# Optimization experiments

Hardware: AMD Instinct MI355X
Metric: run time of the kernel (lower is better)

Reference implementation:

```python
import jax, jax.numpy as jnp
import numpy as np

H = 4            # heads
C = 64           # per-head dim (= hidden, PyG TransformerConv semantics)
HD = 64          # hidden_dim
L = 2            # num_layers
NT = 2           # node types: 0=task, 1=machine
ET = ((0, 1), (1, 0))  # edge types: (src_nt, dst_nt)
N = 16384        # nodes per type (== max_nodes -> simple pos-enc slice)
E = 262144       # edges per edge type


def _ln(x, g, b):
    mu = x.mean(-1, keepdims=True)
    var = ((x - mu) ** 2).mean(-1, keepdims=True)
    return (x - mu) * jax.lax.rsqrt(var + 1e-5) * g + b


def _tconv(x_src, x_dst, ei, Wq, bq, Wk, bk, Wv, bv, Ws, bs, Wb):
    # PyG TransformerConv: heads=H, out_channels=C, concat=False, beta=True
    n_dst = x_dst.shape[0]
    src, dst = ei[0], ei[1]
    q = (x_dst @ Wq + bq).reshape(-1, H, C)
    k = (x_src @ Wk + bk).reshape(-1, H, C)
    v = (x_src @ Wv + bv).reshape(-1, H, C)
    logits = jnp.einsum('ehc,ehc->eh', q[dst], k[src]) * (1.0 / float(np.sqrt(C)))  # [E,H]
    m = jax.ops.segment_max(logits, dst, num_segments=n_dst)          # [N,H] segment softmax
    ex = jnp.exp(logits - m[dst])
    denom = jax.ops.segment_sum(ex, dst, num_segments=n_dst)
    alpha = ex / denom[dst]                                            # [E,H]
    msg = (alpha[:, :, None] * v[src]).reshape(-1, H * C)              # [E,H*C]
    out = jax.ops.segment_sum(msg, dst, num_segments=n_dst)
    out = out.reshape(n_dst, H, C).mean(axis=1)                        # concat=False -> head mean
    r = x_dst @ Ws + bs                                                # lin_skip
    beta = jax.nn.sigmoid(jnp.concatenate([out, r, out - r], -1) @ Wb) # lin_beta, [N,1]
    return beta * r + (1.0 - beta) * out


def _forward(edge_index, x, W_in, b_in, type_emb, pos, Wq, bq, Wk, bk, Wv, bv,
             Wskip, bskip, Wbeta, ln_g, ln_b, ff_W1, ff_b1, ff_W2, ff_b2, W_out, b_out):
    # input proj + type embedding + positional encoding (num_nodes == max_nodes -> slice)
    h = [x[t] @ W_in[t] + b_in[t] + type_emb[t] + pos[t] for t in range(NT)]
    for l in range(L):
        hn = [jnp.zeros_like(h[0]), jnp.zeros_like(h[1])]
        for e, (s, d) in enumerate(ET):  # HeteroConv, aggr='sum'
            hn[d] = hn[d] + _tconv(h[s], h[d], edge_index[e],
                                   Wq[l, e], bq[l, e], Wk[l, e], bk[l, e],
                                   Wv[l, e], bv[l, e], Wskip[l, e], bskip[l, e], Wbeta[l, e])
        for t in range(NT):
            hr = _ln(h[t] + hn[t], ln_g[l, t], ln_b[l, t])
            ff = jax.nn.gelu(hr @ ff_W1[l, t] + ff_b1[l, t], approximate=False) @ ff_W2[l, t] + ff_b2[l, t]
            h[t] = hr + ff
    return jnp.stack([h[t] @ W_out[t] + b_out[t] for t in range(NT)])  # [NT,N,HD]


def setup_inputs() -> dict:
    key = jax.random.key(0)
    ks = jax.random.split(key, 16)
    w = lambda k, s: 0.02 * jax.random.normal(k, s, jnp.float32)
    NE = len(ET)
    return {
        'x': jax.random.normal(ks[0], (NT, N, HD), jnp.float32),
        'edge_index': jax.random.randint(ks[1], (NE, 2, E), 0, N, jnp.int32),
        'W_in': w(ks[2], (NT, HD, HD)), 'b_in': jnp.zeros((NT, HD), jnp.float32),
        'type_emb': w(ks[3], (NT, HD)),
        'pos': w(ks[4], (NT, N, HD)),
        'Wq': w(ks[5], (L, NE, HD, H * C)), 'bq': jnp.zeros((L, NE, H * C), jnp.float32),
        'Wk': w(ks[6], (L, NE, HD, H * C)), 'bk': jnp.zeros((L, NE, H * C), jnp.float32),
        'Wv': w(ks[7], (L, NE, HD, H * C)), 'bv': jnp.zeros((L, NE, H * C), jnp.float32),
        'Wskip': w(ks[8], (L, NE, HD, HD)), 'bskip': jnp.zeros((L, NE, HD), jnp.float32),
        'Wbeta': w(ks[9], (L, NE, 3 * HD, 1)),
        'ln_g': jnp.ones((L, NT, HD), jnp.float32), 'ln_b': jnp.zeros((L, NT, HD), jnp.float32),
        'ff_W1': w(ks[10], (L, NT, HD, 4 * HD)), 'ff_b1': jnp.zeros((L, NT, 4 * HD), jnp.float32),
        'ff_W2': w(ks[11], (L, NT, 4 * HD, HD)), 'ff_b2': jnp.zeros((L, NT, HD), jnp.float32),
        'W_out': w(ks[12], (NT, HD, HD)), 'b_out': jnp.zeros((NT, HD), jnp.float32),
    }


def reference(x, edge_index, W_in, b_in, type_emb, pos, Wq, bq, Wk, bk, Wv, bv,
              Wskip, bskip, Wbeta, ln_g, ln_b, ff_W1, ff_b1, ff_W2, ff_b2, W_out, b_out):
    return _forward(edge_index, x, W_in, b_in, type_emb, pos, Wq, bq, Wk, bk, Wv, bv,
                    Wskip, bskip, Wbeta, ln_g, ln_b, ff_W1, ff_b1, ff_W2, ff_b2, W_out, b_out)
```

## Files before the change

### kernel.cpp

```cpp
#include <hip/hip_runtime.h>
#include <math.h>

#define NN 16384
#define EE 262144

typedef __bf16 v8bf __attribute__((ext_vector_type(8)));
typedef __bf16 v4bf __attribute__((ext_vector_type(4)));
typedef float  v4f  __attribute__((ext_vector_type(4)));
typedef float  v2f  __attribute__((ext_vector_type(2)));

#define OFF_CNT     0
#define OFF_FILL    (2*NN)
#define OFF_ROWPTR  (4*NN)
#define OFF_COLSRC  98816
#define OFF_H       623104
#define OFF_HN      (OFF_H  + 2*NN*64)
#define OFF_Q       (OFF_HN + 2*NN*64)
#define OFF_KV      (OFF_Q  + 2*NN*128)
#define OFF_R       (OFF_KV + 2*NN*128)

__device__ __forceinline__ float blo(unsigned u) { return __uint_as_float(u << 16); }
__device__ __forceinline__ float bhi(unsigned u) { return __uint_as_float(u & 0xffff0000u); }
__device__ __forceinline__ unsigned short f2b(float f) {
  __bf16 h = (__bf16)f;
  return *(unsigned short*)&h;
}

__global__ void count_kernel(const int* __restrict__ ei, int* __restrict__ cnt) {
  int idx = blockIdx.x * 256 + threadIdx.x;
  if (idx >= 2 * EE) return;
  int et = idx >> 18;
  int j  = idx & (EE - 1);
  int dst = ei[et * 2 * EE + EE + j];
  atomicAdd(&cnt[et * NN + dst], 1);
}

__global__ __launch_bounds__(1024) void scan_kernel(const int* __restrict__ cnt,
                                                    int* __restrict__ rowptr,
                                                    int* __restrict__ fill) {
  int et = blockIdx.x;
  const int* c = cnt + et * NN;
  __shared__ int sums[1024];
  int tid = threadIdx.x;
  int base = tid * 16;
  int loc[16];
  int s = 0;
#pragma unroll
  for (int i = 0; i < 16; ++i) { loc[i] = s; s += c[base + i]; }
  sums[tid] = s;
  __syncthreads();
  for (int off = 1; off < 1024; off <<= 1) {
    int v = 0;
    if (tid >= off) v = sums[tid - off];
    __syncthreads();
    if (tid >= off) sums[tid] += v;
    __syncthreads();
  }
  int ebase = (tid == 0) ? 0 : sums[tid - 1];
  int* rp = rowptr + et * (NN + 1);
  int* fl = fill + et * NN;
#pragma unroll
  for (int i = 0; i < 16; ++i) {
    rp[base + i] = ebase + loc[i];
    fl[base + i] = ebase + loc[i];
  }
  if (tid == 1023) rp[NN] = sums[1023];
}

__global__ void scatter_kernel(const int* __restrict__ ei, int* __restrict__ fill,
                               int* __restrict__ colsrc) {
  int idx = blockIdx.x * 256 + threadIdx.x;
  if (idx >= 2 * EE) return;
  int et = idx >> 18;
  int j  = idx & (EE - 1);
  int src = ei[et * 2 * EE + j];
  int dst = ei[et * 2 * EE + EE + j];
  int pos = atomicAdd(&fill[et * NN + dst], 1);
  colsrc[et * EE + pos] = (et * NN + src) << 9;
}

struct GemmDesc {
  const float *A, *B, *bias, *bias2, *add;
  char* C;
  int Ncols, Cld, ntiles, gelu, otype;
};
struct GemmPack { GemmDesc d[8]; int nd; };

#define LDA 72

__global__ __launch_bounds__(256) void gemm_mfma(GemmPack p) {
  GemmDesc g = p.d[blockIdx.y];
  const int row0 = blockIdx.x * 128;
  const int tid = threadIdx.x;
  const int w = tid >> 6, lane = tid & 63;
  const int l16 = lane & 15, quad = lane >> 4;

  __shared__ __bf16 As[128 * LDA];
  __shared__ __bf16 Bs[64 * LDA];

#pragma unroll
  for (int it = 0; it < 8; ++it) {
    int fi = it * 256 + tid;
    int grow = fi >> 4;
    int kq = (fi & 15) << 2;
    float4 a = *(const float4*)(g.A + (size_t)(row0 + grow) * 64 + kq);
    v4bf c = { (__bf16)a.x, (__bf16)a.y, (__bf16)a.z, (__bf16)a.w };
    *(v4bf*)&As[grow * LDA + kq] = c;
  }

  for (int ct0 = 0; ct0 < g.ntiles; ++ct0) {
    const int col0 = ct0 * 64;
    __syncthreads();
#pragma unroll
    for (int it = 0; it < 4; ++it) {
      int fi = it * 256 + tid;
      int kk = fi >> 4;
      int nq = (fi & 15) << 2;
      float4 b = *(const float4*)(g.B + (size_t)kk * g.Ncols + col0 + nq);
      Bs[(nq + 0) * LDA + kk] = (__bf16)b.x;
      Bs[(nq + 1) * LDA + kk] = (__bf16)b.y;
      Bs[(nq + 2) * LDA + kk] = (__bf16)b.z;
      Bs[(nq + 3) * LDA + kk] = (__bf16)b.w;
    }
    __syncthreads();

    v4f acc[2][4];
#pragma unroll
    for (int rt = 0; rt < 2; ++rt)
#pragma unroll
      for (int ct = 0; ct < 4; ++ct)
#pragma unroll
        for (int r = 0; r < 4; ++r) acc[rt][ct][r] = 0.f;

#pragma unroll
    for (int ks = 0; ks < 2; ++ks) {
      v8bf a0 = *(v8bf*)&As[(w * 32 + l16) * LDA + ks * 32 + quad * 8];
      v8bf a1 = *(v8bf*)&As[(w * 32 + 16 + l16) * LDA + ks * 32 + quad * 8];
#pragma unroll
      for (int ct = 0; ct < 4; ++ct) {
        v8bf bb = *(v8bf*)&Bs[(ct * 16 + l16) * LDA + ks * 32 + quad * 8];
        acc[0][ct] = __builtin_amdgcn_mfma_f32_16x16x32_bf16(a0, bb, acc[0][ct], 0, 0, 0);
        acc[1][ct] = __builtin_amdgcn_mfma_f32_16x16x32_bf16(a1, bb, acc[1][ct], 0, 0, 0);
      }
    }

    float bias_c[4];
#pragma unroll
    for (int ct = 0; ct < 4; ++ct) {
      int col = col0 + ct * 16 + l16;
      float b = g.bias ? g.bias[col] : 0.f;
      if (g.bias2) b += g.bias2[col];
      bias_c[ct] = b;
    }
#pragma unroll
    for (int rt = 0; rt < 2; ++rt)
#pragma unroll
      for (int r = 0; r < 4; ++r) {
        size_t row = row0 + w * 32 + rt * 16 + quad * 4 + r;
        char* cp = g.C + row * (size_t)g.Cld;
#pragma unroll
        for (int ct = 0; ct < 4; ++ct) {
          int col = col0 + ct * 16 + l16;
          float v = acc[rt][ct][r] + bias_c[ct];
          if (g.add) v += g.add[row * g.Ncols + col];
          if (g.gelu) v = 0.5f * v * (1.f + erff(v * 0.70710678118654752f));
          if (g.otype == 0)      *(float*)(cp + col * 4) = v;
          else if (g.otype == 1) *(unsigned short*)(cp + col * 2) = f2b(v);
          else {
            unsigned pk = __builtin_amdgcn_cvt_pk_fp8_f32(v, v, 0, false);
            *(unsigned char*)(cp + col) = (unsigned char)(pk & 0xff);
          }
        }
      }
  }
}

struct FFPack {
  const float *HN, *W1, *b1, *W2, *b2;
  float* H;
  const float *Wout, *bout;
  float* outbuf;
};

__global__ __launch_bounds__(256) void ff_fused(FFPack p) {
  const int t = blockIdx.y;
  const int row0 = blockIdx.x * 64;
  const int tid = threadIdx.x;
  const int w = tid >> 6, lane = tid & 63;
  const int l16 = lane & 15, quad = lane >> 4;

  const float* A  = p.HN + ((size_t)t * NN) * 64;
  const float* W1 = p.W1 + (size_t)t * 64 * 256;
  const float* b1 = p.b1 + t * 256;
  const float* W2 = p.W2 + (size_t)t * 256 * 64;
  const float* b2 = p.b2 + t * 64;

  __shared__ __bf16 As[64 * LDA];
  __shared__ __bf16 A2[64 * LDA];
  __shared__ __bf16 B1s[64 * LDA];
  __shared__ __bf16 B2s[64 * LDA];

#pragma unroll
  for (int it = 0; it < 4; ++it) {
    int fi = it * 256 + tid;
    int grow = fi >> 4;
    int kq = (fi & 15) << 2;
    float4 a = *(const float4*)(A + (size_t)(row0 + grow) * 64 + kq);
    v4bf c = { (__bf16)a.x, (__bf16)a.y, (__bf16)a.z, (__bf16)a.w };
    *(v4bf*)&As[grow * LDA + kq] = c;
  }

  v4f acc2[4];
#pragma unroll
  for (int ct = 0; ct < 4; ++ct)
#pragma unroll
    for (int r = 0; r < 4; ++r) acc2[ct][r] = 0.f;

  for (int c1 = 0; c1 < 4; ++c1) {
#pragma unroll
    for (int it = 0; it < 4; ++it) {
      int fi = it * 256 + tid;
      int kk = fi >> 4;
      int nq = (fi & 15) << 2;
      float4 b = *(const float4*)(W1 + (size_t)kk * 256 + c1 * 64 + nq);
      B1s[(nq + 0) * LDA + kk] = (__bf16)b.x;
      B1s[(nq + 1) * LDA + kk] = (__bf16)b.y;
      B1s[(nq + 2) * LDA + kk] = (__bf16)b.z;
      B1s[(nq + 3) * LDA + kk] = (__bf16)b.w;
      float4 b2v = *(const float4*)(W2 + (size_t)(c1 * 64 + kk) * 64 + nq);
      B2s[(nq + 0) * LDA + kk] = (__bf16)b2v.x;
      B2s[(nq + 1) * LDA + kk] = (__bf16)b2v.y;
      B2s[(nq + 2) * LDA + kk] = (__bf16)b2v.z;
      B2s[(nq + 3) * LDA + kk] = (__bf16)b2v.w;
    }
    __syncthreads();

    v4f acc1[4];
#pragma unroll
    for (int ct = 0; ct < 4; ++ct)
#pragma unroll
      for (int r = 0; r < 4; ++r) acc1[ct][r] = 0.f;
#pragma unroll
    for (int ks = 0; ks < 2; ++ks) {
      v8bf a = *(v8bf*)&As[(w * 16 + l16) * LDA + ks * 32 + quad * 8];
#pragma unroll
      for (int ct = 0; ct < 4; ++ct) {
        v8bf bb = *(v8bf*)&B1s[(ct * 16 + l16) * LDA + ks * 32 + quad * 8];
        acc1[ct] = __builtin_amdgcn_mfma_f32_16x16x32_bf16(a, bb, acc1[ct], 0, 0, 0);
      }
    }
#pragma unroll
    for (int ct = 0; ct < 4; ++ct) {
      float bb = b1[c1 * 64 + ct * 16 + l16];
#pragma unroll
      for (int r = 0; r < 4; ++r) {
        float v = acc1[ct][r] + bb;
        v = 0.5f * v * (1.f + erff(v * 0.70710678118654752f));
        A2[(w * 16 + quad * 4 + r) * LDA + ct * 16 + l16] = (__bf16)v;
      }
    }
#pragma unroll
    for (int ks = 0; ks < 2; ++ks) {
      v8bf a = *(v8bf*)&A2[(w * 16 + l16) * LDA + ks * 32 + quad * 8];
#pragma unroll
      for (int ct = 0; ct < 4; ++ct) {
        v8bf bb = *(v8bf*)&B2s[(ct * 16 + l16) * LDA + ks * 32 + quad * 8];
        acc2[ct] = __builtin_amdgcn_mfma_f32_16x16x32_bf16(a, bb, acc2[ct], 0, 0, 0);
      }
    }
    __syncthreads();
  }

  if (!p.outbuf) {
#pragma unroll
    for (int ct = 0; ct < 4; ++ct) {
      int col = ct * 16 + l16;
      float bb = b2[col];
#pragma unroll
      for (int r = 0; r < 4; ++r) {
        size_t row = (size_t)t * NN + row0 + w * 16 + quad * 4 + r;
        float v = acc2[ct][r] + bb + p.HN[row * 64 + col];
        p.H[row * 64 + col] = v;
      }
    }
    return;
  }

#pragma unroll
  for (int ct = 0; ct < 4; ++ct) {
    int col = ct * 16 + l16;
    float bb = b2[col];
#pragma unroll
    for (int r = 0; r < 4; ++r) {
      int lrow = w * 16 + quad * 4 + r;
      size_t row = (size_t)t * NN + row0 + lrow;
      float v = acc2[ct][r] + bb + p.HN[row * 64 + col];
      A2[lrow * LDA + col] = (__bf16)v;
    }
  }
  {
    const float* Wo = p.Wout + (size_t)t * 64 * 64;
#pragma unroll
    for (int it = 0; it < 4; ++it) {
      int fi = it * 256 + tid;
      int kk = fi >> 4;
      int nq = (fi & 15) << 2;
      float4 b = *(const float4*)(Wo + (size_t)kk * 64 + nq);
      B1s[(nq + 0) * LDA + kk] = (__bf16)b.x;
      B1s[(nq + 1) * LDA + kk] = (__bf16)b.y;
      B1s[(nq + 2) * LDA + kk] = (__bf16)b.z;
      B1s[(nq + 3) * LDA + kk] = (__bf16)b.w;
    }
  }
  __syncthreads();

  v4f acc3[4];
#pragma unroll
  for (int ct = 0; ct < 4; ++ct)
#pragma unroll
    for (int r = 0; r < 4; ++r) acc3[ct][r] = 0.f;
#pragma unroll
  for (int ks = 0; ks < 2; ++ks) {
    v8bf a = *(v8bf*)&A2[(w * 16 + l16) * LDA + ks * 32 + quad * 8];
#pragma unroll
    for (int ct = 0; ct < 4; ++ct) {
      v8bf bb = *(v8bf*)&B1s[(ct * 16 + l16) * LDA + ks * 32 + quad * 8];
      acc3[ct] = __builtin_amdgcn_mfma_f32_16x16x32_bf16(a, bb, acc3[ct], 0, 0, 0);
    }
  }
  const float* bo = p.bout + t * 64;
#pragma unroll
  for (int ct = 0; ct < 4; ++ct) {
    int col = ct * 16 + l16;
    float bb = bo[col];
#pragma unroll
    for (int r = 0; r < 4; ++r) {
      size_t row = (size_t)t * NN + row0 + w * 16 + quad * 4 + r;
      p.outbuf[row * 64 + col] = acc3[ct][r] + bb;
    }
  }
}

struct AggPack {
  const unsigned short *Q;
  const char *KV;
  const float *R;
  const float *Wb;
  const float *Hin;
  const float *lng, *lnb;
  float* outHR;
  const int *rowptr;
  const int *colsrc;
};

__global__ __launch_bounds__(256) void agg_kernel(AggPack p) {
  const int et = blockIdx.y, d = 1 - et;
  int wid = __builtin_amdgcn_readfirstlane(threadIdx.x >> 6);
  int lane = threadIdx.x & 63;
  int node = blockIdx.x * 4 + wid;
  int c4 = lane & 15;
  int cb = ((lane >> 4) << 6) + (c4 << 2);

  const int* rp = p.rowptr + et * (NN + 1);
  const int* cs = p.colsrc + et * EE;
  int start = rp[node], end = rp[node + 1];
  int len = end - start;
  int gnode = d * NN + node;

  uint2 qw = *(const uint2*)(p.Q + ((size_t)gnode << 8) + cb);
  float q0 = blo(qw.x) * 0.125f, q1 = bhi(qw.x) * 0.125f;
  float q2 = blo(qw.y) * 0.125f, q3 = bhi(qw.y) * 0.125f;

  int b[5];
#pragma unroll
  for (int i = 0; i <= 4; ++i) b[i] = start + ((len * i) >> 2);
  float dsum[4] = {0.f, 0.f, 0.f, 0.f};
  float acc[4][4];
#pragma unroll
  for (int s4 = 0; s4 < 4; ++s4)
#pragma unroll
    for (int c = 0; c < 4; ++c) acc[s4][c] = 0.f;

  int maxn = (len + 3) >> 2;
  int last = end - 1;
  for (int it = 0; it < maxn; ++it) {
#pragma unroll
    for (int s4 = 0; s4 < 4; ++s4) {
      int j = b[s4] + it;
      bool act = j < b[s4 + 1];
      int jc = act ? j : last;
      int off = cs[jc];
      const char* rowp = p.KV + off;
      unsigned kw = *(const unsigned*)(rowp + cb);
      unsigned vw = *(const unsigned*)(rowp + 256 + cb);
      v2f kl = __builtin_amdgcn_cvt_pk_f32_fp8((int)kw, false);
      v2f kh = __builtin_amdgcn_cvt_pk_f32_fp8((int)kw, true);
      float pd = q0 * kl[0] + q1 * kl[1] + q2 * kh[0] + q3 * kh[1];
      pd += __shfl_xor(pd, 1);
      pd += __shfl_xor(pd, 2);
      pd += __shfl_xor(pd, 4);
      pd += __shfl_xor(pd, 8);
      float wgt = act ? __expf(pd) : 0.f;
      v2f vl = __builtin_amdgcn_cvt_pk_f32_fp8((int)vw, false);
      v2f vh = __builtin_amdgcn_cvt_pk_f32_fp8((int)vw, true);
      dsum[s4] += wgt;
      acc[s4][0] += wgt * vl[0];
      acc[s4][1] += wgt * vl[1];
      acc[s4][2] += wgt * vh[0];
      acc[s4][3] += wgt * vh[1];
    }
  }
  float dn = (dsum[0] + dsum[1]) + (dsum[2] + dsum[3]);
  float ax = (acc[0][0] + acc[1][0]) + (acc[2][0] + acc[3][0]);
  float ay = (acc[0][1] + acc[1][1]) + (acc[2][1] + acc[3][1]);
  float az = (acc[0][2] + acc[1][2]) + (acc[2][2] + acc[3][2]);
  float aw = (acc[0][3] + acc[1][3]) + (acc[2][3] + acc[3][3]);

  float inv = (len > 0) ? (0.25f / dn) : 0.f;
  float ox = ax * inv, oy = ay * inv, oz = az * inv, ow = aw * inv;
  ox += __shfl_xor(ox, 16); ox += __shfl_xor(ox, 32);
  oy += __shfl_xor(oy, 16); oy += __shfl_xor(oy, 32);
  oz += __shfl_xor(oz, 16); oz += __shfl_xor(oz, 32);
  ow += __shfl_xor(ow, 16); ow += __shfl_xor(ow, 32);

  int cc = c4 << 2;
  float4 r = *(const float4*)(p.R + (size_t)gnode * 64 + cc);
  const float* wb = p.Wb + et * 192;
  float part = ox * wb[cc] + oy * wb[cc + 1] + oz * wb[cc + 2] + ow * wb[cc + 3]
             + r.x * wb[64 + cc] + r.y * wb[64 + cc + 1]
             + r.z * wb[64 + cc + 2] + r.w * wb[64 + cc + 3]
             + (ox - r.x) * wb[128 + cc] + (oy - r.y) * wb[128 + cc + 1]
             + (oz - r.z) * wb[128 + cc + 2] + (ow - r.w) * wb[128 + cc + 3];
  part += __shfl_xor(part, 1);
  part += __shfl_xor(part, 2);
  part += __shfl_xor(part, 4);
  part += __shfl_xor(part, 8);
  float beta = 1.f / (1.f + __expf(-part));

  float4 hv = *(const float4*)(p.Hin + (size_t)gnode * 64 + cc);
  float yx = hv.x + beta * r.x + (1.f - beta) * ox;
  float yy = hv.y + beta * r.y + (1.f - beta) * oy;
  float yz = hv.z + beta * r.z + (1.f - beta) * oz;
  float yw = hv.w + beta * r.w + (1.f - beta) * ow;
  float sa = yx + yy + yz + yw;
  float sb = yx * yx + yy * yy + yz * yz + yw * yw;
  sa += __shfl_xor(sa, 1); sb += __shfl_xor(sb, 1);
  sa += __shfl_xor(sa, 2); sb += __shfl_xor(sb, 2);
  sa += __shfl_xor(sa, 4); sb += __shfl_xor(sb, 4);
  sa += __shfl_xor(sa, 8); sb += __shfl_xor(sb, 8);
  float mu = sa * (1.f / 64.f);
  float var = sb * (1.f / 64.f) - mu * mu;
  float rs = rsqrtf(var + 1e-5f);
  if (lane < 16) {
    const float* lng = p.lng + d * 64;
    const float* lnb = p.lnb + d * 64;
    float4 gg = *(const float4*)(lng + cc);
    float4 bb = *(const float4*)(lnb + cc);
    float4 res;
    res.x = (yx - mu) * rs * gg.x + bb.x;
    res.y = (yy - mu) * rs * gg.y + bb.y;
    res.z = (yz - mu) * rs * gg.z + bb.z;
    res.w = (yw - mu) * rs * gg.w + bb.w;
    *(float4*)(p.outHR + (size_t)gnode * 64 + cc) = res;
  }
}

static void add_desc(GemmPack& p, const float* A, const float* B,
                     const float* bias, const float* bias2, const float* add,
                     void* C, int Nc, int Cld, int gelu, int otype) {
  GemmDesc& g = p.d[p.nd++];
  g.A = A; g.B = B; g.bias = bias; g.bias2 = bias2; g.add = add; g.C = (char*)C;
  g.Ncols = Nc; g.Cld = Cld; g.ntiles = Nc / 64;
  g.gelu = gelu; g.otype = otype;
}

extern "C" void kernel_launch(void* const* d_in, const int* in_sizes, int n_in,
                              void* d_out, int out_size, void* d_ws, size_t ws_size,
                              hipStream_t stream) {
  const float* x        = (const float*)d_in[0];
  const int*   ei       = (const int*)d_in[1];
  const float* W_in     = (const float*)d_in[2];
  const float* b_in     = (const float*)d_in[3];
  const float* type_emb = (const float*)d_in[4];
  const float* pos      = (const float*)d_in[5];
  const float* Wq       = (const float*)d_in[6];
  const float* bq       = (const float*)d_in[7];
  const float* Wk       = (const float*)d_in[8];
  const float* bk       = (const float*)d_in[9];
  const float* Wv       = (const float*)d_in[10];
  const float* bv       = (const float*)d_in[11];
  const float* Wskip    = (const float*)d_in[12];
  const float* bskip    = (const float*)d_in[13];
  const float* Wbeta    = (const float*)d_in[14];
  const float* ln_g     = (const float*)d_in[15];
  const float* ln_b     = (const float*)d_in[16];
  const float* ff_W1    = (const float*)d_in[17];
  const float* ff_b1    = (const float*)d_in[18];
  const float* ff_W2    = (const float*)d_in[19];
  const float* ff_b2    = (const float*)d_in[20];
  const float* W_out    = (const float*)d_in[21];
  const float* b_out    = (const float*)d_in[22];
  float* out = (float*)d_out;

  int*   wsi = (int*)d_ws;
  float* wsf = (float*)d_ws;
  int* cnt    = wsi + OFF_CNT;
  int* fill   = wsi + OFF_FILL;
  int* rowptr = wsi + OFF_ROWPTR;
  int* colsrc = wsi + OFF_COLSRC;
  float* H  = wsf + OFF_H;
  float* HN = wsf + OFF_HN;
  unsigned short* Qb = (unsigned short*)(wsf + OFF_Q);
  char* KVb = (char*)(wsf + OFF_KV);
  float* Rb = wsf + OFF_R;

  hipMemsetAsync(cnt, 0, 2 * NN * sizeof(int), stream);
  count_kernel<<<dim3(2 * EE / 256), dim3(256), 0, stream>>>(ei, cnt);
  scan_kernel<<<dim3(2), dim3(1024), 0, stream>>>(cnt, rowptr, fill);
  scatter_kernel<<<dim3(2 * EE / 256), dim3(256), 0, stream>>>(ei, fill, colsrc);

  {
    GemmPack p{};
    for (int t = 0; t < 2; ++t)
      add_desc(p, x + (size_t)t * NN * 64, W_in + t * 64 * 64,
               b_in + t * 64, type_emb + t * 64, pos + (size_t)t * NN * 64,
               H + (size_t)t * NN * 64, 64, 256, 0, 0);
    gemm_mfma<<<dim3(128, p.nd), dim3(256), 0, stream>>>(p);
  }

  for (int l = 0; l < 2; ++l) {
    {
      GemmPack p{};
      for (int et = 0; et < 2; ++et) {
        int s = et, d = 1 - et;
        int we = l * 2 + et;
        const float* hs = H + (size_t)s * NN * 64;
        const float* hd = H + (size_t)d * NN * 64;
        add_desc(p, hd, Wq + (size_t)we * 64 * 256, bq + we * 256,
                 nullptr, nullptr, (char*)Qb + (size_t)d * NN * 512, 256, 512, 0, 1);
        add_desc(p, hs, Wk + (size_t)we * 64 * 256, bk + we * 256,
                 nullptr, nullptr, KVb + (size_t)s * NN * 512, 256, 512, 0, 2);
        add_desc(p, hs, Wv + (size_t)we * 64 * 256, bv + we * 256,
                 nullptr, nullptr, KVb + (size_t)s * NN * 512 + 256, 256, 512, 0, 2);
        add_desc(p, hd, Wskip + (size_t)we * 64 * 64, bskip + we * 64,
                 nullptr, nullptr, Rb + (size_t)d * NN * 64, 64, 256, 0, 0);
      }
      gemm_mfma<<<dim3(128, p.nd), dim3(256), 0, stream>>>(p);
    }

    AggPack ap;
    ap.Q = Qb; ap.KV = KVb; ap.R = Rb;
    ap.Wb = Wbeta + l * 2 * 192;
    ap.Hin = H;
    ap.lng = ln_g + l * 128;
    ap.lnb = ln_b + l * 128;
    ap.outHR = HN;
    ap.rowptr = rowptr;
    ap.colsrc = colsrc;
    agg_kernel<<<dim3(NN / 4, 2), dim3(256), 0, stream>>>(ap);

    FFPack fp;
    fp.HN = HN;
    fp.W1 = ff_W1 + (size_t)l * 2 * 64 * 256;
    fp.b1 = ff_b1 + l * 2 * 256;
    fp.W2 = ff_W2 + (size_t)l * 2 * 256 * 64;
    fp.b2 = ff_b2 + l * 2 * 64;
    fp.H  = H;
    fp.Wout = W_out;
    fp.bout = b_out;
    fp.outbuf = (l == 1) ? out : nullptr;
    ff_fused<<<dim3(NN / 64, 2), dim3(256), 0, stream>>>(fp);
  }
}
```

Baseline: 368.4 us.

## Interleave K and V fp8 rows and gather 16-byte chunks per lane in aggregation

The GEMM epilogue now writes K and V fp8 values interleaved in 8-byte groups, so each 16-byte chunk of a KV row holds 8 K values followed by the matching 8 V values. The aggregation kernel processes two edges per wave, one per half-wave, and each lane loads one 16-byte KV chunk instead of two separate 4-byte K and V loads. The next edge's column index is prefetched a step ahead. The intent is fewer, wider gather loads and a shorter shuffle reduction per edge. The cost is more register accumulators and a larger cross-lane reduction at the end.

Measured after the change: 378.6 us. 1.03x slower.

```diff
diff --git a/kernel.cpp b/kernel.cpp
--- a/kernel.cpp
+++ b/kernel.cpp
@@ -168,7 +168,8 @@
           else if (g.otype == 1) *(unsigned short*)(cp + col * 2) = f2b(v);
           else {
             unsigned pk = __builtin_amdgcn_cvt_pk_fp8_f32(v, v, 0, false);
-            *(unsigned char*)(cp + col) = (unsigned char)(pk & 0xff);
+            int boff = ((col >> 3) << 4) + (col & 7) + ((g.otype == 3) ? 8 : 0);
+            *(unsigned char*)(cp + boff) = (unsigned char)(pk & 0xff);
           }
         }
       }
@@ -358,8 +359,8 @@
   int wid = __builtin_amdgcn_readfirstlane(threadIdx.x >> 6);
   int lane = threadIdx.x & 63;
   int node = blockIdx.x * 4 + wid;
-  int c4 = lane & 15;
-  int cb = ((lane >> 4) << 6) + (c4 << 2);
+  int lh = lane & 31;
+  int half = lane >> 5;
 
   const int* rp = p.rowptr + et * (NN + 1);
   const int* cs = p.colsrc + et * EE;
@@ -367,101 +368,158 @@
   int len = end - start;
   int gnode = d * NN + node;
 
-  uint2 qw = *(const uint2*)(p.Q + ((size_t)gnode << 8) + cb);
+  uint4 qw = *(const uint4*)(p.Q + ((size_t)gnode << 8) + lh * 8);
   float q0 = blo(qw.x) * 0.125f, q1 = bhi(qw.x) * 0.125f;
   float q2 = blo(qw.y) * 0.125f, q3 = bhi(qw.y) * 0.125f;
-
-  int b[5];
-#pragma unroll
-  for (int i = 0; i <= 4; ++i) b[i] = start + ((len * i) >> 2);
-  float dsum[4] = {0.f, 0.f, 0.f, 0.f};
-  float acc[4][4];
-#pragma unroll
-  for (int s4 = 0; s4 < 4; ++s4)
-#pragma unroll
-    for (int c = 0; c < 4; ++c) acc[s4][c] = 0.f;
+  float q4 = blo(qw.z) * 0.125f, q5 = bhi(qw.z) * 0.125f;
+  float q6 = blo(qw.w) * 0.125f, q7 = bhi(qw.w) * 0.125f;
+
+  int mid = start + (len >> 1);
+  int last = end - 1;
+  float dsum0 = 0.f, dsum1 = 0.f;
+  float acc0[8], acc1[8];
+#pragma unroll
+  for (int i = 0; i < 8; ++i) { acc0[i] = 0.f; acc1[i] = 0.f; }
 
   int maxn = (len + 3) >> 2;
-  int last = end - 1;
+  int j0 = start + half, j1 = mid + half;
+  bool a0 = j0 < mid, a1 = j1 < end;
+  int o0 = 0, o1 = 0;
+  if (len > 0) {
+    o0 = cs[a0 ? j0 : last];
+    o1 = cs[a1 ? j1 : last];
+  }
+  int lb = lh * 16;
   for (int it = 0; it < maxn; ++it) {
-#pragma unroll
-    for (int s4 = 0; s4 < 4; ++s4) {
-      int j = b[s4] + it;
-      bool act = j < b[s4 + 1];
-      int jc = act ? j : last;
-      int off = cs[jc];
-      const char* rowp = p.KV + off;
-      unsigned kw = *(const unsigned*)(rowp + cb);
-      unsigned vw = *(const unsigned*)(rowp + 256 + cb);
-      v2f kl = __builtin_amdgcn_cvt_pk_f32_fp8((int)kw, false);
-      v2f kh = __builtin_amdgcn_cvt_pk_f32_fp8((int)kw, true);
-      float pd = q0 * kl[0] + q1 * kl[1] + q2 * kh[0] + q3 * kh[1];
+    uint4 kv0 = *(const uint4*)(p.KV + (size_t)(o0 + lb));
+    uint4 kv1 = *(const uint4*)(p.KV + (size_t)(o1 + lb));
+    float w0 = a0 ? 1.f : 0.f;
+    float w1 = a1 ? 1.f : 0.f;
+    j0 += 2; j1 += 2;
+    a0 = j0 < mid; a1 = j1 < end;
+    o0 = cs[a0 ? j0 : last];
+    o1 = cs[a1 ? j1 : last];
+
+    {
+      v2f ka = __builtin_amdgcn_cvt_pk_f32_fp8((int)kv0.x, false);
+      v2f kb = __builtin_amdgcn_cvt_pk_f32_fp8((int)kv0.x, true);
+      v2f kc = __builtin_amdgcn_cvt_pk_f32_fp8((int)kv0.y, false);
+      v2f kd = __builtin_amdgcn_cvt_pk_f32_fp8((int)kv0.y, true);
+      float pd = q0 * ka[0] + q1 * ka[1] + q2 * kb[0] + q3 * kb[1]
+               + q4 * kc[0] + q5 * kc[1] + q6 * kd[0] + q7 * kd[1];
       pd += __shfl_xor(pd, 1);
       pd += __shfl_xor(pd, 2);
       pd += __shfl_xor(pd, 4);
-      pd += __shfl_xor(pd, 8);
-      float wgt = act ? __expf(pd) : 0.f;
-      v2f vl = __builtin_amdgcn_cvt_pk_f32_fp8((int)vw, false);
-      v2f vh = __builtin_amdgcn_cvt_pk_f32_fp8((int)vw, true);
-      dsum[s4] += wgt;
-      acc[s4][0] += wgt * vl[0];
-      acc[s4][1] += wgt * vl[1];
-      acc[s4][2] += wgt * vh[0];
-      acc[s4][3] += wgt * vh[1];
-    }
-  }
-  float dn = (dsum[0] + dsum[1]) + (dsum[2] + dsum[3]);
-  float ax = (acc[0][0] + acc[1][0]) + (acc[2][0] + acc[3][0]);
-  float ay = (acc[0][1] + acc[1][1]) + (acc[2][1] + acc[3][1]);
-  float az = (acc[0][2] + acc[1][2]) + (acc[2][2] + acc[3][2]);
-  float aw = (acc[0][3] + acc[1][3]) + (acc[2][3] + acc[3][3]);
-
+      float wgt = w0 * __expf(pd);
+      v2f va = __builtin_amdgcn_cvt_pk_f32_fp8((int)kv0.z, false);
+      v2f vb = __builtin_amdgcn_cvt_pk_f32_fp8((int)kv0.z, true);
+      v2f vc = __builtin_amdgcn_cvt_pk_f32_fp8((int)kv0.w, false);
+      v2f vd = __builtin_amdgcn_cvt_pk_f32_fp8((int)kv0.w, true);
+      dsum0 += wgt;
+      acc0[0] += wgt * va[0]; acc0[1] += wgt * va[1];
+      acc0[2] += wgt * vb[0]; acc0[3] += wgt * vb[1];
+      acc0[4] += wgt * vc[0]; acc0[5] += wgt * vc[1];
+      acc0[6] += wgt * vd[0]; acc0[7] += wgt * vd[1];
+    }
+    {
+      v2f ka = __builtin_amdgcn_cvt_pk_f32_fp8((int)kv1.x, false);
+      v2f kb = __builtin_amdgcn_cvt_pk_f32_fp8((int)kv1.x, true);
+      v2f kc = __builtin_amdgcn_cvt_pk_f32_fp8((int)kv1.y, false);
+      v2f kd = __builtin_amdgcn_cvt_pk_f32_fp8((int)kv1.y, true);
+      float pd = q0 * ka[0] + q1 * ka[1] + q2 * kb[0] + q3 * kb[1]
+               + q4 * kc[0] + q5 * kc[1] + q6 * kd[0] + q7 * kd[1];
+      pd += __shfl_xor(pd, 1);
+      pd += __shfl_xor(pd, 2);
+      pd += __shfl_xor(pd, 4);
+      float wgt = w1 * __expf(pd);
+      v2f va = __builtin_amdgcn_cvt_pk_f32_fp8((int)kv1.z, false);
+      v2f vb = __builtin_amdgcn_cvt_pk_f32_fp8((int)kv1.z, true);
+      v2f vc = __builtin_amdgcn_cvt_pk_f32_fp8((int)kv1.w, false);
+      v2f vd = __builtin_amdgcn_cvt_pk_f32_fp8((int)kv1.w, true);
+      dsum1 += wgt;
+      acc1[0] += wgt * va[0]; acc1[1] += wgt * va[1];
+      acc1[2] += wgt * vb[0]; acc1[3] += wgt * vb[1];
+      acc1[4] += wgt * vc[0]; acc1[5] += wgt * vc[1];
+      acc1[6] += wgt * vd[0]; acc1[7] += wgt * vd[1];
+    }
+  }
+
+  float dn = dsum0 + dsum1;
+  dn += __shfl_xor(dn, 32);
   float inv = (len > 0) ? (0.25f / dn) : 0.f;
-  float ox = ax * inv, oy = ay * inv, oz = az * inv, ow = aw * inv;
-  ox += __shfl_xor(ox, 16); ox += __shfl_xor(ox, 32);
-  oy += __shfl_xor(oy, 16); oy += __shfl_xor(oy, 32);
-  oz += __shfl_xor(oz, 16); oz += __shfl_xor(oz, 32);
-  ow += __shfl_xor(ow, 16); ow += __shfl_xor(ow, 32);
-
-  int cc = c4 << 2;
-  float4 r = *(const float4*)(p.R + (size_t)gnode * 64 + cc);
+
+  float o_[8];
+#pragma unroll
+  for (int i = 0; i < 8; ++i) {
+    float a = acc0[i] + acc1[i];
+    a += __shfl_xor(a, 32);
+    a *= inv;
+    a += __shfl_xor(a, 8);
+    a += __shfl_xor(a, 16);
+    o_[i] = a;
+  }
+
+  int cc = (lane & 7) << 3;
+  const float* rptr = p.R + (size_t)gnode * 64 + cc;
+  float4 r0 = *(const float4*)(rptr);
+  float4 r1 = *(const float4*)(rptr + 4);
+  float rr[8] = { r0.x, r0.y, r0.z, r0.w, r1.x, r1.y, r1.z, r1.w };
+
   const float* wb = p.Wb + et * 192;
-  float part = ox * wb[cc] + oy * wb[cc + 1] + oz * wb[cc + 2] + ow * wb[cc + 3]
-             + r.x * wb[64 + cc] + r.y * wb[64 + cc + 1]
-             + r.z * wb[64 + cc + 2] + r.w * wb[64 + cc + 3]
-             + (ox - r.x) * wb[128 + cc] + (oy - r.y) * wb[128 + cc + 1]
-             + (oz - r.z) * wb[128 + cc + 2] + (ow - r.w) * wb[128 + cc + 3];
+  float4 wo0 = *(const float4*)(wb + cc),       wo1 = *(const float4*)(wb + cc + 4);
+  float4 wr0 = *(const float4*)(wb + 64 + cc),  wr1 = *(const float4*)(wb + 64 + cc + 4);
+  float4 wd0 = *(const float4*)(wb + 128 + cc), wd1 = *(const float4*)(wb + 128 + cc + 4);
+  float wov[8] = { wo0.x, wo0.y, wo0.z, wo0.w, wo1.x, wo1.y, wo1.z, wo1.w };
+  float wrv[8] = { wr0.x, wr0.y, wr0.z, wr0.w, wr1.x, wr1.y, wr1.z, wr1.w };
+  float wdv[8] = { wd0.x, wd0.y, wd0.z, wd0.w, wd1.x, wd1.y, wd1.z, wd1.w };
+  float part = 0.f;
+#pragma unroll
+  for (int i = 0; i < 8; ++i)
+    part += o_[i] * wov[i] + rr[i] * wrv[i] + (o_[i] - rr[i]) * wdv[i];
   part += __shfl_xor(part, 1);
   part += __shfl_xor(part, 2);
   part += __shfl_xor(part, 4);
-  part += __shfl_xor(part, 8);
   float beta = 1.f / (1.f + __expf(-part));
 
-  float4 hv = *(const float4*)(p.Hin + (size_t)gnode * 64 + cc);
-  float yx = hv.x + beta * r.x + (1.f - beta) * ox;
-  float yy = hv.y + beta * r.y + (1.f - beta) * oy;
-  float yz = hv.z + beta * r.z + (1.f - beta) * oz;
-  float yw = hv.w + beta * r.w + (1.f - beta) * ow;
-  float sa = yx + yy + yz + yw;
-  float sb = yx * yx + yy * yy + yz * yz + yw * yw;
+  const float* hptr = p.Hin + (size_t)gnode * 64 + cc;
+  float4 h0 = *(const float4*)(hptr);
+  float4 h1 = *(const float4*)(hptr + 4);
+  float hh[8] = { h0.x, h0.y, h0.z, h0.w, h1.x, h1.y, h1.z, h1.w };
+  float y[8];
+  float sa = 0.f, sb = 0.f;
+#pragma unroll
+  for (int i = 0; i < 8; ++i) {
+    float v = hh[i] + beta * rr[i] + (1.f - beta) * o_[i];
+    y[i] = v;
+    sa += v;
+    sb += v * v;
+  }
   sa += __shfl_xor(sa, 1); sb += __shfl_xor(sb, 1);
   sa += __shfl_xor(sa, 2); sb += __shfl_xor(sb, 2);
   sa += __shfl_xor(sa, 4); sb += __shfl_xor(sb, 4);
-  sa += __shfl_xor(sa, 8); sb += __shfl_xor(sb, 8);
   float mu = sa * (1.f / 64.f);
   float var = sb * (1.f / 64.f) - mu * mu;
   float rs = rsqrtf(var + 1e-5f);
-  if (lane < 16) {
-    const float* lng = p.lng + d * 64;
-    const float* lnb = p.lnb + d * 64;
-    float4 gg = *(const float4*)(lng + cc);
-    float4 bb = *(const float4*)(lnb + cc);
-    float4 res;
-    res.x = (yx - mu) * rs * gg.x + bb.x;
-    res.y = (yy - mu) * rs * gg.y + bb.y;
-    res.z = (yz - mu) * rs * gg.z + bb.z;
-    res.w = (yw - mu) * rs * gg.w + bb.w;
-    *(float4*)(p.outHR + (size_t)gnode * 64 + cc) = res;
+
+  if (lane < 8) {
+    const float* lng = p.lng + d * 64 + cc;
+    const float* lnb = p.lnb + d * 64 + cc;
+    float4 g0 = *(const float4*)(lng);
+    float4 g1 = *(const float4*)(lng + 4);
+    float4 bb0 = *(const float4*)(lnb);
+    float4 bb1 = *(const float4*)(lnb + 4);
+    float4 res0, res1;
+    res0.x = (y[0] - mu) * rs * g0.x + bb0.x;
+    res0.y = (y[1] - mu) * rs * g0.y + bb0.y;
+    res0.z = (y[2] - mu) * rs * g0.z + bb0.z;
+    res0.w = (y[3] - mu) * rs * g0.w + bb0.w;
+    res1.x = (y[4] - mu) * rs * g1.x + bb1.x;
+    res1.y = (y[5] - mu) * rs * g1.y + bb1.y;
+    res1.z = (y[6] - mu) * rs * g1.z + bb1.z;
+    res1.w = (y[7] - mu) * rs * g1.w + bb1.w;
+    float* op = p.outHR + (size_t)gnode * 64 + cc;
+    *(float4*)(op) = res0;
+    *(float4*)(op + 4) = res1;
   }
 }
 
@@ -541,7 +599,7 @@
         add_desc(p, hs, Wk + (size_t)we * 64 * 256, bk + we * 256,
                  nullptr, nullptr, KVb + (size_t)s * NN * 512, 256, 512, 0, 2);
         add_desc(p, hs, Wv + (size_t)we * 64 * 256, bv + we * 256,
-                 nullptr, nullptr, KVb + (size_t)s * NN * 512 + 256, 256, 512, 0, 2);
+                 nullptr, nullptr, KVb + (size_t)s * NN * 512, 256, 512, 0, 3);
         add_desc(p, hd, Wskip + (size_t)we * 64 * 64, bskip + we * 64,
                  nullptr, nullptr, Rb + (size_t)d * NN * 64, 64, 256, 0, 0);
       }
```
